# Kernel optimization log

Measured on AMD Instinct MI355X. Metric: run time of the kernel, lower is better.

Reference implementation:

```python
import jax, jax.numpy as jnp
import numpy as np

NUM_CELLS = 2048
CELL_DIM = 256
N_STATES = 131072


def setup_inputs() -> dict:
    key = jax.random.key(0)
    k1, k2 = jax.random.split(key)
    x = jax.random.normal(k1, (N_STATES, CELL_DIM), dtype=jnp.float32)
    placeCells = jax.random.normal(k2, (NUM_CELLS, CELL_DIM), dtype=jnp.float32)
    return {"x": x, "placeCells": placeCells}


def reference(x, placeCells):
    # states: (N, cellDim); sims: (N, numCells); output: (N,) int argmax
    states = x.reshape(-1, CELL_DIM)
    sims = jnp.matmul(states, placeCells.T)  # (N, numCells) dense similarity
    return jnp.argmax(sims, axis=1)
```

## Files before the change

kernel.cpp:

```cpp
#include <hip/hip_runtime.h>
#include <float.h>
#include <stdint.h>

#define NUM_CELLS 2048
#define CELL_DIM  256
#define N_STATES  131072

typedef _Float16 half8 __attribute__((ext_vector_type(8)));
typedef float    f32x4 __attribute__((ext_vector_type(4)));

#define M1 0.10f
#define M2 0.0008f
#define CAP1 32768
#define CAP2 4096

#define WS_C1 0
#define WS_C2 4
#define WS_L1 1024
#define WS_L2 (WS_L1 + 4 * CAP1)
#define WS_PH 262144
#define WS_PL (WS_PH + 1048576)
#define WS_NEEDED (WS_PL + 1048576 + 131072)

__global__ void prep_p(const float* __restrict__ p, _Float16* __restrict__ ph,
                       _Float16* __restrict__ pl, int* __restrict__ c1,
                       int* __restrict__ c2) {
    int d = blockIdx.x * 256 + threadIdx.x;
    if (d == 0) { *c1 = 0; *c2 = 0; }
    int l = d & 63, kf = (d >> 6) & 7, ct = d >> 9;
    int cell = ct * 16 + (l & 15);
    int k0 = kf * 32 + (l >> 4) * 8;
    const float* s = p + cell * 256 + k0;
    float4 a = *(const float4*)s, b = *(const float4*)(s + 4);
    float v[8] = {a.x, a.y, a.z, a.w, b.x, b.y, b.z, b.w};
    half8 h, lo;
#pragma unroll
    for (int j = 0; j < 8; ++j) {
        _Float16 hi = (_Float16)v[j];
        h[j] = hi;
        lo[j] = (_Float16)((v[j] - (float)hi) * 2048.0f);
    }
    *(half8*)(ph + (size_t)d * 8) = h;
    *(half8*)(pl + (size_t)d * 8) = lo;
}

__launch_bounds__(512, 2)
__global__ void pc_gemm1(const float* __restrict__ x, const _Float16* __restrict__ ph,
                         int* __restrict__ out, int* __restrict__ c1,
                         int* __restrict__ l1) {
    __shared__ _Float16 smem[32768];

    const int tid = threadIdx.x;
    const int l = tid & 63;
    const int w = tid >> 6;
    const int wr = w >> 2, wc = w & 3;

    const float* xg = x + (size_t)blockIdx.x * (128 * CELL_DIM);
#pragma unroll
    for (int i = 0; i < 8; ++i) {
        int d = tid + i * 512;
        int dl = d & 63, kf = (d >> 6) & 7, rt = d >> 9;
        int row = rt * 16 + (dl & 15);
        int k0 = kf * 32 + (dl >> 4) * 8;
        const float* s = xg + row * 256 + k0;
        float4 a = *(const float4*)s, b = *(const float4*)(s + 4);
        half8 h;
        h[0] = (_Float16)a.x; h[1] = (_Float16)a.y;
        h[2] = (_Float16)a.z; h[3] = (_Float16)a.w;
        h[4] = (_Float16)b.x; h[5] = (_Float16)b.y;
        h[6] = (_Float16)b.z; h[7] = (_Float16)b.w;
        *(half8*)(smem + d * 8) = h;
    }
    __syncthreads();

    half8 A[4][8];
#pragma unroll
    for (int rt = 0; rt < 4; ++rt)
#pragma unroll
        for (int kf = 0; kf < 8; ++kf)
            A[rt][kf] = *(const half8*)(smem + (((wr * 4 + rt) * 8 + kf) * 64 + l) * 8);
    __syncthreads();

    const _Float16* bb = ph + wc * 4096 + (size_t)l * 8;

    half8 Bf[4];
    Bf[0] = *(const half8*)(bb + 0);
    Bf[1] = *(const half8*)(bb + 512);
    Bf[2] = *(const half8*)(bb + 1024);
    Bf[3] = *(const half8*)(bb + 1536);

    float t1[16], t2[16];
    int ic[16];
#pragma unroll
    for (int s = 0; s < 16; ++s) { t1[s] = -FLT_MAX; t2[s] = -FLT_MAX; ic[s] = 0; }

    for (int t = 0; t < 32; ++t) {
        const _Float16* bt = bb + t * 16384;
        f32x4 a0 = {}, a1 = {}, a2 = {}, a3 = {};
#pragma unroll
        for (int k = 0; k < 8; ++k) {
            half8 B = Bf[k & 3];
            Bf[k & 3] = *(const half8*)(bt + ((k < 4) ? (k + 4) * 512
                                                      : (16384 + (k - 4) * 512)));
            a0 = __builtin_amdgcn_mfma_f32_16x16x32_f16(A[0][k], B, a0, 0, 0, 0);
            a1 = __builtin_amdgcn_mfma_f32_16x16x32_f16(A[1][k], B, a1, 0, 0, 0);
            a2 = __builtin_amdgcn_mfma_f32_16x16x32_f16(A[2][k], B, a2, 0, 0, 0);
            a3 = __builtin_amdgcn_mfma_f32_16x16x32_f16(A[3][k], B, a3, 0, 0, 0);
        }
#define UPD(ACC, RT)                                                       \
        _Pragma("unroll")                                                  \
        for (int reg = 0; reg < 4; ++reg) {                                \
            int s = (RT) * 4 + reg;                                        \
            float v = (ACC)[reg];                                          \
            float nt2 = __builtin_amdgcn_fmed3f(t1[s], t2[s], v);          \
            ic[s] = (v > t1[s]) ? t : ic[s];                               \
            t1[s] = fmaxf(t1[s], v);                                       \
            t2[s] = nt2;                                                   \
        }
        UPD(a0, 0) UPD(a1, 1) UPD(a2, 2) UPD(a3, 3)
#undef UPD
    }

    int idx[16];
#pragma unroll
    for (int s = 0; s < 16; ++s) idx[s] = (ic[s] * 4 + wc) * 16 + (l & 15);
#pragma unroll
    for (int m = 1; m <= 8; m <<= 1) {
#pragma unroll
        for (int s = 0; s < 16; ++s) {
            float ot1 = __shfl_xor(t1[s], m, 64);
            int   oi  = __shfl_xor(idx[s], m, 64);
            float ot2 = __shfl_xor(t2[s], m, 64);
            float nt2 = fmaxf(fminf(t1[s], ot1), fmaxf(t2[s], ot2));
            if (ot1 > t1[s] || (ot1 == t1[s] && oi < idx[s])) { t1[s] = ot1; idx[s] = oi; }
            t2[s] = nt2;
        }
    }

    float* rT1 = (float*)smem;
    int*   rI1 = (int*)smem + 512;
    float* rT2 = (float*)smem + 1024;
    if ((l & 15) == 0) {
#pragma unroll
        for (int rt = 0; rt < 4; ++rt)
#pragma unroll
            for (int reg = 0; reg < 4; ++reg) {
                int s = rt * 4 + reg;
                int row = wr * 64 + rt * 16 + (l >> 4) * 4 + reg;
                rT1[row * 4 + wc] = t1[s];
                rI1[row * 4 + wc] = idx[s];
                rT2[row * 4 + wc] = t2[s];
            }
    }
    __syncthreads();
    if (tid < 128) {
        float T1 = -FLT_MAX, T2 = -FLT_MAX; int I1 = 0x7FFFFFFF;
#pragma unroll
        for (int g = 0; g < 4; ++g) {
            float v1 = rT1[tid * 4 + g];
            int   vi = rI1[tid * 4 + g];
            float v2 = rT2[tid * 4 + g];
            float nt2 = fmaxf(fminf(T1, v1), fmaxf(T2, v2));
            if (v1 > T1 || (v1 == T1 && vi < I1)) { T1 = v1; I1 = vi; }
            T2 = nt2;
        }
        int grow = blockIdx.x * 128 + tid;
        out[grow] = I1;
        if (T1 - T2 < M1) {
            int pos = atomicAdd(c1, 1);
            if (pos < CAP1) l1[pos] = grow;
        }
    }
}

__launch_bounds__(256, 2)
__global__ void pc_rescue2(const float* __restrict__ x, const _Float16* __restrict__ ph,
                           const _Float16* __restrict__ pl,
                           const int* __restrict__ c1, const int* __restrict__ l1,
                           int* __restrict__ out, int* __restrict__ c2,
                           int* __restrict__ l2) {
    const int n0 = *c1;
    const int n = n0 < CAP1 ? n0 : CAP1;
    const int base = blockIdx.x * 16;
    if (base >= n) return;
    const int tid = threadIdx.x;
    const int l = tid & 63, wc = tid >> 6;

    const int rslot = base + (l & 15);
    const int my_row = l1[rslot < n ? rslot : (n - 1)];

    half8 Ah[8], Al[8];
#pragma unroll
    for (int kf = 0; kf < 8; ++kf) {
        const float* s = x + (size_t)my_row * 256 + kf * 32 + (l >> 4) * 8;
        float4 a = *(const float4*)s, b = *(const float4*)(s + 4);
        float v[8] = {a.x, a.y, a.z, a.w, b.x, b.y, b.z, b.w};
#pragma unroll
        for (int j = 0; j < 8; ++j) {
            _Float16 hi = (_Float16)v[j];
            Ah[kf][j] = hi;
            Al[kf][j] = (_Float16)((v[j] - (float)hi) * 2048.0f);
        }
    }

    const _Float16* bh = ph + wc * 4096 + (size_t)l * 8;
    const _Float16* bl = pl + wc * 4096 + (size_t)l * 8;
    half8 BH[4], BL[4];
#pragma unroll
    for (int j = 0; j < 4; ++j) {
        BH[j] = *(const half8*)(bh + j * 512);
        BL[j] = *(const half8*)(bl + j * 512);
    }

    float t1[4], t2[4];
    int ic[4];
#pragma unroll
    for (int s = 0; s < 4; ++s) { t1[s] = -FLT_MAX; t2[s] = -FLT_MAX; ic[s] = 0; }

    for (int t = 0; t < 32; ++t) {
        const _Float16* bth = bh + t * 16384;
        const _Float16* btl = bl + t * 16384;
        f32x4 hh = {}, hl = {}, lh = {};
#pragma unroll
        for (int k = 0; k < 8; ++k) {
            half8 Bh_ = BH[k & 3], Bl_ = BL[k & 3];
            int off = (k < 4) ? (k + 4) * 512 : (16384 + (k - 4) * 512);
            BH[k & 3] = *(const half8*)(bth + off);
            BL[k & 3] = *(const half8*)(btl + off);
            hh = __builtin_amdgcn_mfma_f32_16x16x32_f16(Ah[k], Bh_, hh, 0, 0, 0);
            hl = __builtin_amdgcn_mfma_f32_16x16x32_f16(Ah[k], Bl_, hl, 0, 0, 0);
            lh = __builtin_amdgcn_mfma_f32_16x16x32_f16(Al[k], Bh_, lh, 0, 0, 0);
        }
#pragma unroll
        for (int reg = 0; reg < 4; ++reg) {
            float v = hh[reg] + (hl[reg] + lh[reg]) * (1.0f / 2048.0f);
            float nt2 = __builtin_amdgcn_fmed3f(t1[reg], t2[reg], v);
            ic[reg] = (v > t1[reg]) ? t : ic[reg];
            t1[reg] = fmaxf(t1[reg], v);
            t2[reg] = nt2;
        }
    }

    int idx[4];
#pragma unroll
    for (int s = 0; s < 4; ++s) idx[s] = (ic[s] * 4 + wc) * 16 + (l & 15);
#pragma unroll
    for (int m = 1; m <= 8; m <<= 1) {
#pragma unroll
        for (int s = 0; s < 4; ++s) {
            float ot1 = __shfl_xor(t1[s], m, 64);
            int   oi  = __shfl_xor(idx[s], m, 64);
            float ot2 = __shfl_xor(t2[s], m, 64);
            float nt2 = fmaxf(fminf(t1[s], ot1), fmaxf(t2[s], ot2));
            if (ot1 > t1[s] || (ot1 == t1[s] && oi < idx[s])) { t1[s] = ot1; idx[s] = oi; }
            t2[s] = nt2;
        }
    }

    __shared__ float rT1[64];
    __shared__ int   rI1[64];
    __shared__ float rT2[64];
    if ((l & 15) == 0) {
#pragma unroll
        for (int reg = 0; reg < 4; ++reg) {
            int r = (l >> 4) * 4 + reg;
            rT1[r * 4 + wc] = t1[reg];
            rI1[r * 4 + wc] = idx[reg];
            rT2[r * 4 + wc] = t2[reg];
        }
    }
    __syncthreads();
    if (tid < 16) {
        float T1 = -FLT_MAX, T2 = -FLT_MAX; int I1 = 0x7FFFFFFF;
#pragma unroll
        for (int g = 0; g < 4; ++g) {
            float v1 = rT1[tid * 4 + g];
            int   vi = rI1[tid * 4 + g];
            float v2 = rT2[tid * 4 + g];
            float nt2 = fmaxf(fminf(T1, v1), fmaxf(T2, v2));
            if (v1 > T1 || (v1 == T1 && vi < I1)) { T1 = v1; I1 = vi; }
            T2 = nt2;
        }
        int slot = base + tid;
        if (slot < n) {
            int grow = l1[slot];
            out[grow] = I1;
            if (T1 - T2 < M2) {
                int pos = atomicAdd(c2, 1);
                if (pos < CAP2) l2[pos] = grow;
            }
        }
    }
}

__global__ void rescue3(const float* __restrict__ x, const float* __restrict__ p,
                        const int* __restrict__ count, const int* __restrict__ list,
                        int* __restrict__ out) {
    __shared__ float xrow[256];
    __shared__ float pch[32][260];
    __shared__ float red2[32][9];
    __shared__ float bvs[32];
    __shared__ int   bis[32];
    const int tid = threadIdx.x;
    const int n0 = *count;
    const int n = n0 < CAP2 ? n0 : CAP2;
    for (int e = blockIdx.x; e < n; e += gridDim.x) {
        const int row = list[e];
        __syncthreads();
        if (tid < 64) {
            float4 v = *(const float4*)(x + (size_t)row * 256 + tid * 4);
            *(float4*)(&xrow[tid * 4]) = v;
        }
        float bv = -FLT_MAX; int bi = 0;
        const int cell = tid & 31, kq = tid >> 5;
        for (int c0 = 0; c0 < NUM_CELLS; c0 += 32) {
            __syncthreads();
#pragma unroll
            for (int i = 0; i < 8; ++i) {
                int f = tid + i * 256;
                int cr = f >> 6, k4 = (f & 63) * 4;
                float4 v = *(const float4*)(p + (size_t)(c0 + cr) * 256 + k4);
                *(float4*)(&pch[cr][k4]) = v;
            }
            __syncthreads();
            float s = 0.f;
#pragma unroll
            for (int j = 0; j < 8; ++j) {
                float4 pv = *(const float4*)(&pch[cell][kq * 32 + j * 4]);
                float4 xv = *(const float4*)(&xrow[kq * 32 + j * 4]);
                s = fmaf(xv.x, pv.x, s); s = fmaf(xv.y, pv.y, s);
                s = fmaf(xv.z, pv.z, s); s = fmaf(xv.w, pv.w, s);
            }
            red2[cell][kq] = s;
            __syncthreads();
            if (tid < 32) {
                float dot = 0.f;
#pragma unroll
                for (int q = 0; q < 8; ++q) dot += red2[tid][q];
                if (dot > bv) { bv = dot; bi = c0 + tid; }
            }
        }
        if (tid < 32) { bvs[tid] = bv; bis[tid] = bi; }
        __syncthreads();
        if (tid == 0) {
            float B = bvs[0]; int BI = bis[0];
#pragma unroll
            for (int t = 1; t < 32; ++t)
                if (bvs[t] > B || (bvs[t] == B && bis[t] < BI)) { B = bvs[t]; BI = bis[t]; }
            out[row] = BI;
        }
    }
}

#define BM 64
#define BN 64
#define BK 32
#define XP 260
#define PP 68
__launch_bounds__(256, 2)
__global__ void placecells_argmax_fp32(const float* __restrict__ x,
                                       const float* __restrict__ pc,
                                       int* __restrict__ out) {
    __shared__ float xs[BM * XP];
    __shared__ float ps[BK * PP];
    const int tid = threadIdx.x;
    const int tx = tid & 15;
    const int ty = tid >> 4;
    const float* xg = x + (size_t)blockIdx.x * (BM * CELL_DIM);
#pragma unroll
    for (int i = 0; i < 16; ++i) {
        int f = tid + i * 256;
        int s = f >> 6, k4 = (f & 63) << 2;
        *(float4*)(&xs[s * XP + k4]) = *(const float4*)(xg + s * CELL_DIM + k4);
    }
    __syncthreads();
    float runv[4]; int runi[4];
#pragma unroll
    for (int si = 0; si < 4; ++si) { runv[si] = -FLT_MAX; runi[si] = 0; }
    for (int jc = 0; jc < NUM_CELLS; jc += BN) {
        float acc[4][4];
#pragma unroll
        for (int si = 0; si < 4; ++si)
#pragma unroll
            for (int cj = 0; cj < 4; ++cj) acc[si][cj] = 0.0f;
        for (int kc = 0; kc < CELL_DIM; kc += BK) {
            __syncthreads();
#pragma unroll
            for (int i = 0; i < 2; ++i) {
                int f = tid + i * 256;
                int c = f >> 3, k4 = (f & 7) << 2;
                float4 v = *(const float4*)(pc + (size_t)(jc + c) * CELL_DIM + kc + k4);
                ps[(k4 + 0) * PP + c] = v.x; ps[(k4 + 1) * PP + c] = v.y;
                ps[(k4 + 2) * PP + c] = v.z; ps[(k4 + 3) * PP + c] = v.w;
            }
            __syncthreads();
#pragma unroll
            for (int kk = 0; kk < BK; kk += 4) {
                float4 xv[4];
#pragma unroll
                for (int si = 0; si < 4; ++si)
                    xv[si] = *(const float4*)(&xs[(ty * 4 + si) * XP + kc + kk]);
#pragma unroll
                for (int kt = 0; kt < 4; ++kt) {
                    float4 pv = *(const float4*)(&ps[(kk + kt) * PP + tx * 4]);
#pragma unroll
                    for (int si = 0; si < 4; ++si) {
                        float xk = (kt == 0) ? xv[si].x : (kt == 1) ? xv[si].y :
                                   (kt == 2) ? xv[si].z : xv[si].w;
                        acc[si][0] = fmaf(xk, pv.x, acc[si][0]);
                        acc[si][1] = fmaf(xk, pv.y, acc[si][1]);
                        acc[si][2] = fmaf(xk, pv.z, acc[si][2]);
                        acc[si][3] = fmaf(xk, pv.w, acc[si][3]);
                    }
                }
            }
        }
#pragma unroll
        for (int si = 0; si < 4; ++si)
#pragma unroll
            for (int cj = 0; cj < 4; ++cj) {
                int idx = jc + tx * 4 + cj;
                if (acc[si][cj] > runv[si]) { runv[si] = acc[si][cj]; runi[si] = idx; }
            }
    }
    __syncthreads();
    float* rv = ps; int* ri = (int*)(ps + 1024);
#pragma unroll
    for (int si = 0; si < 4; ++si) {
        int s = ty * 4 + si;
        rv[s * 16 + tx] = runv[si]; ri[s * 16 + tx] = runi[si];
    }
    __syncthreads();
    if (tid < BM) {
        float bv = rv[tid * 16]; int bi = ri[tid * 16];
#pragma unroll
        for (int t = 1; t < 16; ++t) {
            float v = rv[tid * 16 + t]; int i = ri[tid * 16 + t];
            if (v > bv || (v == bv && i < bi)) { bv = v; bi = i; }
        }
        out[(size_t)blockIdx.x * BM + tid] = bi;
    }
}

extern "C" void kernel_launch(void* const* d_in, const int* in_sizes, int n_in,
                              void* d_out, int out_size, void* d_ws, size_t ws_size,
                              hipStream_t stream) {
    const float* x  = (const float*)d_in[0];
    const float* pc = (const float*)d_in[1];
    int* out = (int*)d_out;

    if (ws_size >= (size_t)WS_NEEDED) {
        char* ws = (char*)d_ws;
        int* c1 = (int*)(ws + WS_C1);
        int* c2 = (int*)(ws + WS_C2);
        int* l1 = (int*)(ws + WS_L1);
        int* l2 = (int*)(ws + WS_L2);
        _Float16* ph = (_Float16*)(ws + WS_PH);
        _Float16* pl = (_Float16*)(ws + WS_PL);
        prep_p<<<256, 256, 0, stream>>>(pc, ph, pl, c1, c2);
        pc_gemm1<<<N_STATES / 128, 512, 0, stream>>>(x, ph, out, c1, l1);
        pc_rescue2<<<CAP1 / 16, 256, 0, stream>>>(x, ph, pl, c1, l1, out, c2, l2);
        rescue3<<<128, 256, 0, stream>>>(x, pc, c2, l2, out);
    } else {
        placecells_argmax_fp32<<<N_STATES / BM, 256, 0, stream>>>(x, pc, out);
    }
}
```

Measured before the change: 514.7 us.

## Deepen B prefetch, aggregate atomics per wave, persist rescue grid

pc_gemm1 now loads x with nontemporal loads and prefetches the whole next tile's eight B fragments instead of a half-tile rolling buffer, aiming to hide more global-load latency at the cost of extra registers. The flagged-row append now uses one ballot-based atomicAdd per wavefront instead of one per thread, cutting contention on the counter. pc_rescue2 becomes a grid-stride loop over 256 blocks instead of launching CAP1/16 blocks that mostly exit early, and rescue3's grid is halved. The larger register footprint may reduce occupancy under the existing launch bounds.

Result: faster. 501.3 us (-2.6%).

```diff
diff --git a/kernel.cpp b/kernel.cpp
--- a/kernel.cpp
+++ b/kernel.cpp
@@ -8,6 +8,7 @@
 
 typedef _Float16 half8 __attribute__((ext_vector_type(8)));
 typedef float    f32x4 __attribute__((ext_vector_type(4)));
+typedef float    f32x4v __attribute__((ext_vector_type(4)));
 
 #define M1 0.10f
 #define M2 0.0008f
@@ -62,13 +63,14 @@
         int dl = d & 63, kf = (d >> 6) & 7, rt = d >> 9;
         int row = rt * 16 + (dl & 15);
         int k0 = kf * 32 + (dl >> 4) * 8;
-        const float* s = xg + row * 256 + k0;
-        float4 a = *(const float4*)s, b = *(const float4*)(s + 4);
+        const f32x4v* s = (const f32x4v*)(xg + row * 256 + k0);
+        f32x4v a = __builtin_nontemporal_load(s);
+        f32x4v b = __builtin_nontemporal_load(s + 1);
         half8 h;
-        h[0] = (_Float16)a.x; h[1] = (_Float16)a.y;
-        h[2] = (_Float16)a.z; h[3] = (_Float16)a.w;
-        h[4] = (_Float16)b.x; h[5] = (_Float16)b.y;
-        h[6] = (_Float16)b.z; h[7] = (_Float16)b.w;
+        h[0] = (_Float16)a[0]; h[1] = (_Float16)a[1];
+        h[2] = (_Float16)a[2]; h[3] = (_Float16)a[3];
+        h[4] = (_Float16)b[0]; h[5] = (_Float16)b[1];
+        h[6] = (_Float16)b[2]; h[7] = (_Float16)b[3];
         *(half8*)(smem + d * 8) = h;
     }
     __syncthreads();
@@ -83,11 +85,9 @@
 
     const _Float16* bb = ph + wc * 4096 + (size_t)l * 8;
 
-    half8 Bf[4];
-    Bf[0] = *(const half8*)(bb + 0);
-    Bf[1] = *(const half8*)(bb + 512);
-    Bf[2] = *(const half8*)(bb + 1024);
-    Bf[3] = *(const half8*)(bb + 1536);
+    half8 Bf[8];
+#pragma unroll
+    for (int j = 0; j < 8; ++j) Bf[j] = *(const half8*)(bb + j * 512);
 
     float t1[16], t2[16];
     int ic[16];
@@ -95,13 +95,12 @@
     for (int s = 0; s < 16; ++s) { t1[s] = -FLT_MAX; t2[s] = -FLT_MAX; ic[s] = 0; }
 
     for (int t = 0; t < 32; ++t) {
-        const _Float16* bt = bb + t * 16384;
+        const _Float16* bn = bb + (t + 1) * 16384;
         f32x4 a0 = {}, a1 = {}, a2 = {}, a3 = {};
 #pragma unroll
         for (int k = 0; k < 8; ++k) {
-            half8 B = Bf[k & 3];
-            Bf[k & 3] = *(const half8*)(bt + ((k < 4) ? (k + 4) * 512
-                                                      : (16384 + (k - 4) * 512)));
+            half8 B = Bf[k];
+            Bf[k] = *(const half8*)(bn + k * 512);
             a0 = __builtin_amdgcn_mfma_f32_16x16x32_f16(A[0][k], B, a0, 0, 0, 0);
             a1 = __builtin_amdgcn_mfma_f32_16x16x32_f16(A[1][k], B, a1, 0, 0, 0);
             a2 = __builtin_amdgcn_mfma_f32_16x16x32_f16(A[2][k], B, a2, 0, 0, 0);
@@ -166,8 +165,15 @@
         }
         int grow = blockIdx.x * 128 + tid;
         out[grow] = I1;
-        if (T1 - T2 < M1) {
-            int pos = atomicAdd(c1, 1);
+        bool f = (T1 - T2 < M1);
+        unsigned long long msk = __ballot(f);
+        int cnt = __popcll(msk);
+        int prefix = __popcll(msk & ((1ull << l) - 1ull));
+        int bpos = 0;
+        if (l == 0 && cnt) bpos = atomicAdd(c1, cnt);
+        bpos = __shfl(bpos, 0, 64);
+        if (f) {
+            int pos = bpos + prefix;
             if (pos < CAP1) l1[pos] = grow;
         }
     }
@@ -181,113 +187,118 @@
                            int* __restrict__ l2) {
     const int n0 = *c1;
     const int n = n0 < CAP1 ? n0 : CAP1;
-    const int base = blockIdx.x * 16;
-    if (base >= n) return;
+    const int G = (n + 15) >> 4;
     const int tid = threadIdx.x;
     const int l = tid & 63, wc = tid >> 6;
-
-    const int rslot = base + (l & 15);
-    const int my_row = l1[rslot < n ? rslot : (n - 1)];
-
-    half8 Ah[8], Al[8];
-#pragma unroll
-    for (int kf = 0; kf < 8; ++kf) {
-        const float* s = x + (size_t)my_row * 256 + kf * 32 + (l >> 4) * 8;
-        float4 a = *(const float4*)s, b = *(const float4*)(s + 4);
-        float v[8] = {a.x, a.y, a.z, a.w, b.x, b.y, b.z, b.w};
-#pragma unroll
-        for (int j = 0; j < 8; ++j) {
-            _Float16 hi = (_Float16)v[j];
-            Ah[kf][j] = hi;
-            Al[kf][j] = (_Float16)((v[j] - (float)hi) * 2048.0f);
-        }
-    }
-
-    const _Float16* bh = ph + wc * 4096 + (size_t)l * 8;
-    const _Float16* bl = pl + wc * 4096 + (size_t)l * 8;
-    half8 BH[4], BL[4];
-#pragma unroll
-    for (int j = 0; j < 4; ++j) {
-        BH[j] = *(const half8*)(bh + j * 512);
-        BL[j] = *(const half8*)(bl + j * 512);
-    }
-
-    float t1[4], t2[4];
-    int ic[4];
-#pragma unroll
-    for (int s = 0; s < 4; ++s) { t1[s] = -FLT_MAX; t2[s] = -FLT_MAX; ic[s] = 0; }
-
-    for (int t = 0; t < 32; ++t) {
-        const _Float16* bth = bh + t * 16384;
-        const _Float16* btl = bl + t * 16384;
-        f32x4 hh = {}, hl = {}, lh = {};
-#pragma unroll
-        for (int k = 0; k < 8; ++k) {
-            half8 Bh_ = BH[k & 3], Bl_ = BL[k & 3];
-            int off = (k < 4) ? (k + 4) * 512 : (16384 + (k - 4) * 512);
-            BH[k & 3] = *(const half8*)(bth + off);
-            BL[k & 3] = *(const half8*)(btl + off);
-            hh = __builtin_amdgcn_mfma_f32_16x16x32_f16(Ah[k], Bh_, hh, 0, 0, 0);
-            hl = __builtin_amdgcn_mfma_f32_16x16x32_f16(Ah[k], Bl_, hl, 0, 0, 0);
-            lh = __builtin_amdgcn_mfma_f32_16x16x32_f16(Al[k], Bh_, lh, 0, 0, 0);
-        }
-#pragma unroll
-        for (int reg = 0; reg < 4; ++reg) {
-            float v = hh[reg] + (hl[reg] + lh[reg]) * (1.0f / 2048.0f);
-            float nt2 = __builtin_amdgcn_fmed3f(t1[reg], t2[reg], v);
-            ic[reg] = (v > t1[reg]) ? t : ic[reg];
-            t1[reg] = fmaxf(t1[reg], v);
-            t2[reg] = nt2;
-        }
-    }
-
-    int idx[4];
-#pragma unroll
-    for (int s = 0; s < 4; ++s) idx[s] = (ic[s] * 4 + wc) * 16 + (l & 15);
-#pragma unroll
-    for (int m = 1; m <= 8; m <<= 1) {
-#pragma unroll
-        for (int s = 0; s < 4; ++s) {
-            float ot1 = __shfl_xor(t1[s], m, 64);
-            int   oi  = __shfl_xor(idx[s], m, 64);
-            float ot2 = __shfl_xor(t2[s], m, 64);
-            float nt2 = fmaxf(fminf(t1[s], ot1), fmaxf(t2[s], ot2));
-            if (ot1 > t1[s] || (ot1 == t1[s] && oi < idx[s])) { t1[s] = ot1; idx[s] = oi; }
-            t2[s] = nt2;
-        }
-    }
 
     __shared__ float rT1[64];
     __shared__ int   rI1[64];
     __shared__ float rT2[64];
-    if ((l & 15) == 0) {
-#pragma unroll
-        for (int reg = 0; reg < 4; ++reg) {
-            int r = (l >> 4) * 4 + reg;
-            rT1[r * 4 + wc] = t1[reg];
-            rI1[r * 4 + wc] = idx[reg];
-            rT2[r * 4 + wc] = t2[reg];
-        }
-    }
-    __syncthreads();
-    if (tid < 16) {
-        float T1 = -FLT_MAX, T2 = -FLT_MAX; int I1 = 0x7FFFFFFF;
-#pragma unroll
-        for (int g = 0; g < 4; ++g) {
-            float v1 = rT1[tid * 4 + g];
-            int   vi = rI1[tid * 4 + g];
-            float v2 = rT2[tid * 4 + g];
-            float nt2 = fmaxf(fminf(T1, v1), fmaxf(T2, v2));
-            if (v1 > T1 || (v1 == T1 && vi < I1)) { T1 = v1; I1 = vi; }
-            T2 = nt2;
-        }
-        int slot = base + tid;
-        if (slot < n) {
-            int grow = l1[slot];
-            out[grow] = I1;
-            if (T1 - T2 < M2) {
-                int pos = atomicAdd(c2, 1);
-                if (pos < CAP2) l2[pos] = grow;
+
+    for (int g = blockIdx.x; g < G; g += gridDim.x) {
+        const int base = g * 16;
+        __syncthreads();
+
+        const int rslot = base + (l & 15);
+        const int my_row = l1[rslot < n ? rslot : (n - 1)];
+
+        half8 Ah[8], Al[8];
+#pragma unroll
+        for (int kf = 0; kf < 8; ++kf) {
+            const float* s = x + (size_t)my_row * 256 + kf * 32 + (l >> 4) * 8;
+            float4 a = *(const float4*)s, b = *(const float4*)(s + 4);
+            float v[8] = {a.x, a.y, a.z, a.w, b.x, b.y, b.z, b.w};
+#pragma unroll
+            for (int j = 0; j < 8; ++j) {
+                _Float16 hi = (_Float16)v[j];
+                Ah[kf][j] = hi;
+                Al[kf][j] = (_Float16)((v[j] - (float)hi) * 2048.0f);
+            }
+        }
+
+        const _Float16* bh = ph + wc * 4096 + (size_t)l * 8;
+        const _Float16* bl = pl + wc * 4096 + (size_t)l * 8;
+        half8 BH[4], BL[4];
+#pragma unroll
+        for (int j = 0; j < 4; ++j) {
+            BH[j] = *(const half8*)(bh + j * 512);
+            BL[j] = *(const half8*)(bl + j * 512);
+        }
+
+        float t1[4], t2[4];
+        int ic[4];
+#pragma unroll
+        for (int s = 0; s < 4; ++s) { t1[s] = -FLT_MAX; t2[s] = -FLT_MAX; ic[s] = 0; }
+
+        for (int t = 0; t < 32; ++t) {
+            const _Float16* bth = bh + t * 16384;
+            const _Float16* btl = bl + t * 16384;
+            f32x4 hh = {}, hl = {}, lh = {};
+#pragma unroll
+            for (int k = 0; k < 8; ++k) {
+                half8 Bh_ = BH[k & 3], Bl_ = BL[k & 3];
+                int off = (k < 4) ? (k + 4) * 512 : (16384 + (k - 4) * 512);
+                BH[k & 3] = *(const half8*)(bth + off);
+                BL[k & 3] = *(const half8*)(btl + off);
+                hh = __builtin_amdgcn_mfma_f32_16x16x32_f16(Ah[k], Bh_, hh, 0, 0, 0);
+                hl = __builtin_amdgcn_mfma_f32_16x16x32_f16(Ah[k], Bl_, hl, 0, 0, 0);
+                lh = __builtin_amdgcn_mfma_f32_16x16x32_f16(Al[k], Bh_, lh, 0, 0, 0);
+            }
+#pragma unroll
+            for (int reg = 0; reg < 4; ++reg) {
+                float v = hh[reg] + (hl[reg] + lh[reg]) * (1.0f / 2048.0f);
+                float nt2 = __builtin_amdgcn_fmed3f(t1[reg], t2[reg], v);
+                ic[reg] = (v > t1[reg]) ? t : ic[reg];
+                t1[reg] = fmaxf(t1[reg], v);
+                t2[reg] = nt2;
+            }
+        }
+
+        int idx[4];
+#pragma unroll
+        for (int s = 0; s < 4; ++s) idx[s] = (ic[s] * 4 + wc) * 16 + (l & 15);
+#pragma unroll
+        for (int m = 1; m <= 8; m <<= 1) {
+#pragma unroll
+            for (int s = 0; s < 4; ++s) {
+                float ot1 = __shfl_xor(t1[s], m, 64);
+                int   oi  = __shfl_xor(idx[s], m, 64);
+                float ot2 = __shfl_xor(t2[s], m, 64);
+                float nt2 = fmaxf(fminf(t1[s], ot1), fmaxf(t2[s], ot2));
+                if (ot1 > t1[s] || (ot1 == t1[s] && oi < idx[s])) { t1[s] = ot1; idx[s] = oi; }
+                t2[s] = nt2;
+            }
+        }
+
+        if ((l & 15) == 0) {
+#pragma unroll
+            for (int reg = 0; reg < 4; ++reg) {
+                int r = (l >> 4) * 4 + reg;
+                rT1[r * 4 + wc] = t1[reg];
+                rI1[r * 4 + wc] = idx[reg];
+                rT2[r * 4 + wc] = t2[reg];
+            }
+        }
+        __syncthreads();
+        if (tid < 16) {
+            float T1 = -FLT_MAX, T2 = -FLT_MAX; int I1 = 0x7FFFFFFF;
+#pragma unroll
+            for (int q = 0; q < 4; ++q) {
+                float v1 = rT1[tid * 4 + q];
+                int   vi = rI1[tid * 4 + q];
+                float v2 = rT2[tid * 4 + q];
+                float nt2 = fmaxf(fminf(T1, v1), fmaxf(T2, v2));
+                if (v1 > T1 || (v1 == T1 && vi < I1)) { T1 = v1; I1 = vi; }
+                T2 = nt2;
+            }
+            int slot = base + tid;
+            if (slot < n) {
+                int grow = l1[slot];
+                out[grow] = I1;
+                if (T1 - T2 < M2) {
+                    int pos = atomicAdd(c2, 1);
+                    if (pos < CAP2) l2[pos] = grow;
+                }
             }
         }
     }
@@ -459,8 +470,8 @@
         _Float16* pl = (_Float16*)(ws + WS_PL);
         prep_p<<<256, 256, 0, stream>>>(pc, ph, pl, c1, c2);
         pc_gemm1<<<N_STATES / 128, 512, 0, stream>>>(x, ph, out, c1, l1);
-        pc_rescue2<<<CAP1 / 16, 256, 0, stream>>>(x, ph, pl, c1, l1, out, c2, l2);
-        rescue3<<<128, 256, 0, stream>>>(x, pc, c2, l2, out);
+        pc_rescue2<<<256, 256, 0, stream>>>(x, ph, pl, c1, l1, out, c2, l2);
+        rescue3<<<64, 256, 0, stream>>>(x, pc, c2, l2, out);
     } else {
         placecells_argmax_fp32<<<N_STATES / BM, 256, 0, stream>>>(x, pc, out);
     }
```
